# Optimization experiments

Hardware: AMD Instinct MI355X
Metric: run time of the kernel (lower is better)

## Reference

```python
import jax, jax.numpy as jnp
import numpy as np

VOCAB, EMB, H = 50000, 300, 64  # fgian_config: embed_dim=300, hidden_dim=64
POL = 3


def _lstm(x, lens, Wih, Whh, b):
    """Masked unidirectional LSTM (PyTorch gate order i,f,g,o).
    x: [B,T,D]; outputs zero past each sequence's length (packed-LSTM semantics)."""
    B, T, _ = x.shape
    Hh = Whh.shape[1]
    xs = jnp.einsum('btd,gd->btg', x, Wih) + b  # precompute input projection [B,T,4H]

    def step(carry, inp):
        h, c = carry
        xproj, t = inp
        g = xproj + h @ Whh.T
        i, f, gg, o = jnp.split(g, 4, axis=-1)
        i = jax.nn.sigmoid(i); f = jax.nn.sigmoid(f)
        gg = jnp.tanh(gg); o = jax.nn.sigmoid(o)
        c_new = f * c + i * gg
        h_new = o * jnp.tanh(c_new)
        m = (t < lens)[:, None]
        return (jnp.where(m, h_new, h), jnp.where(m, c_new, c)), jnp.where(m, h_new, 0.0)

    h0 = jnp.zeros((B, Hh), x.dtype)
    _, out = jax.lax.scan(step, (h0, h0), (xs.transpose(1, 0, 2), jnp.arange(T)))
    return out.transpose(1, 0, 2)


def _bilstm(x, lens, Wih_f, Whh_f, b_f, Wih_b, Whh_b, b_b):
    B, T, _ = x.shape
    t = jnp.arange(T)
    fwd = _lstm(x, lens, Wih_f, Whh_f, b_f)
    # reverse each sequence within its valid length, run fwd scan, reverse back
    ridx = jnp.clip(lens[:, None] - 1 - t[None, :], 0)  # [B,T]
    x_rev = jnp.take_along_axis(x, ridx[..., None], axis=1)
    bwd_rev = _lstm(x_rev, lens, Wih_b, Whh_b, b_b)
    bwd = jnp.take_along_axis(bwd_rev, ridx[..., None], axis=1)
    bwd = jnp.where((t[None, :] < lens[:, None])[..., None], bwd, 0.0)
    return jnp.concatenate([fwd, bwd], axis=-1)  # [B,T,2H]


def setup_inputs() -> dict:
    key = jax.random.key(0)
    ks = jax.random.split(key, 20)
    s = 0.1
    d = {
        'body_idx': jax.random.randint(ks[0], (128, 512), 0, VOCAB),
        'pun_idx': jax.random.randint(ks[1], (128, 256), 0, VOCAB),
        'emb': jax.random.normal(ks[2], (VOCAB, EMB), jnp.float32) * s,
        'w_u': jax.random.normal(ks[15], (6 * H,), jnp.float32) * s,
        'Wd': jax.random.normal(ks[16], (POL, 4 * H), jnp.float32) * s,
        'bd': jnp.zeros((POL,), jnp.float32),
    }
    names = ['bWih_f', 'bWhh_f', 'bb_f', 'bWih_b', 'bWhh_b', 'bb_b',
             'pWih_f', 'pWhh_f', 'pb_f', 'pWih_b', 'pWhh_b', 'pb_b']
    shapes = [(4 * H, EMB), (4 * H, H), (4 * H,)] * 4
    for i, (n, sh) in enumerate(zip(names, shapes)):
        d[n] = jax.random.normal(ks[3 + i], sh, jnp.float32) * s
    return d


def reference(body_idx, pun_idx, emb,
              bWih_f, bWhh_f, bb_f, bWih_b, bWhh_b, bb_b,
              pWih_f, pWhh_f, pb_f, pWih_b, pWhh_b, pb_b,
              w_u, Wd, bd):
    body_len = jnp.sum(body_idx != 0, axis=1)
    pun_len = jnp.sum(pun_idx != 0, axis=1)
    body_M = _bilstm(emb[body_idx], body_len, bWih_f, bWhh_f, bb_f, bWih_b, bWhh_b, bb_b)  # [B,T,2H]
    pun_M = _bilstm(emb[pun_idx], pun_len, pWih_f, pWhh_f, pb_f, pWih_b, pWhh_b, pb_b)     # [B,P,2H]

    # alignment[b,i,j] = [body_i, pun_j, body_i*pun_j] . w_u  -> fully vectorized
    w1, w2, w3 = jnp.split(w_u, 3)
    align = (jnp.einsum('btd,d->bt', body_M, w1)[:, :, None]
             + jnp.einsum('bpd,d->bp', pun_M, w2)[:, None, :]
             + jnp.einsum('btd,bpd->btp', body_M * w3, pun_M))  # [B,T,P]

    att_b = jax.nn.softmax(align.max(axis=2), axis=1)  # [B,T]
    f_pun2body = jnp.einsum('btd,bt->bd', body_M, att_b)
    att_p = jax.nn.softmax(align.max(axis=1), axis=1)  # [B,P]
    f_body2pun = jnp.einsum('bp,bpd->bd', att_p, pun_M)

    feat = jnp.concatenate([f_pun2body, f_body2pun], axis=1)  # [B,4H]
    return feat @ Wd.T + bd
```

## Files before the change

kernel.cpp:

```cpp
#include <hip/hip_runtime.h>


#define B 128
#define TBODY 512
#define TPUN 256
#define EMB 300
#define EMBP 320
#define VOCAB 50000
#define HID 64
#define G4 256
#define NG 512
#define DM 128

typedef __attribute__((ext_vector_type(8))) short bf16x8;
typedef __attribute__((ext_vector_type(4))) float floatx4;
typedef unsigned short u16;

#define OFF_XPB   0u
#define OFF_XPP   134217728u
#define OFF_BODYM 201326592u
#define OFF_PUNM  234881024u
#define OFF_SMALL 251658240u
#define OFF_ABODY (OFF_XPB + 0u)
#define OFF_APUN  (OFF_XPB + 262144u)
#define OFF_MT    (OFF_XPB + 393216u)
#define OFF_MP    (OFF_XPB + 655360u)
#define OFF_COLP  (OFF_XPB + 786432u)
#define OFF_EMBB  OFF_BODYM
#define OFF_WCB   OFF_PUNM
#define OFF_WCP   (OFF_PUNM + 327680u)
#define OFF_BIASB (OFF_PUNM + 655360u)
#define OFF_BIASP (OFF_PUNM + 657408u)
#define OFF_LENS  OFF_SMALL
#define OFF_FEAT  (OFF_SMALL + 1024u)

__device__ inline u16 f2bf(float v) {
    unsigned int u = __float_as_uint(v);
    unsigned int r = (u + 0x7FFFu + ((u >> 16) & 1u)) >> 16;
    return (u16)r;
}

__device__ inline void gload_lds16(const void* g, void* l) {
    __builtin_amdgcn_global_load_lds(
        (const __attribute__((address_space(1))) unsigned int*)g,
        (__attribute__((address_space(3))) unsigned int*)l, 16, 0, 0);
}

#define QBC(v, gg) __int_as_float(__builtin_amdgcn_update_dpp( \
    0, __float_as_int(v), (gg) * 0x55, 0xF, 0xF, true))

__global__ __launch_bounds__(256) void k_lens(const int* __restrict__ bidx,
                                              const int* __restrict__ pidx,
                                              int* __restrict__ lens) {
    int j = blockIdx.x, tid = threadIdx.x;
    const int* src; int n;
    if (j < B) { src = bidx + (size_t)j * TBODY; n = TBODY; }
    else       { src = pidx + (size_t)(j - B) * TPUN; n = TPUN; }
    int c = 0;
    for (int t = tid; t < n; t += 256) c += (src[t] != 0) ? 1 : 0;
    for (int o = 32; o; o >>= 1) c += __shfl_xor(c, o, 64);
    __shared__ int red[4];
    if ((tid & 63) == 0) red[tid >> 6] = c;
    __syncthreads();
    if (tid == 0) lens[j] = red[0] + red[1] + red[2] + red[3];
}

__global__ __launch_bounds__(256) void k_prep_emb(const float* __restrict__ emb,
                                                  u16* __restrict__ embb) {
    int e4 = (blockIdx.x * 256 + threadIdx.x) * 4;
    int row = e4 / EMBP, d = e4 - row * EMBP;
    u16 o0 = 0, o1 = 0, o2 = 0, o3 = 0;
    if (d < EMB) {
        float4 v = *(const float4*)(emb + (size_t)row * EMB + d);
        o0 = f2bf(v.x); o1 = f2bf(v.y); o2 = f2bf(v.z); o3 = f2bf(v.w);
    }
    ushort4 o = {o0, o1, o2, o3};
    *(ushort4*)(embb + e4) = o;
}

__global__ __launch_bounds__(256) void k_prep_w(
    const float* __restrict__ bWih_f, const float* __restrict__ bWih_b,
    const float* __restrict__ bb_f, const float* __restrict__ bb_b,
    const float* __restrict__ pWih_f, const float* __restrict__ pWih_b,
    const float* __restrict__ pb_f, const float* __restrict__ pb_b,
    u16* __restrict__ Wcb, u16* __restrict__ Wcp,
    float* __restrict__ biasb, float* __restrict__ biasp) {
    int e = blockIdx.x * 256 + threadIdx.x;
    const int WSZ = NG * EMBP;
    if (e < WSZ) {
        int g = e / EMBP, d = e - g * EMBP;
        float v = 0.f;
        if (d < EMB) v = (g < G4) ? bWih_f[g * EMB + d] : bWih_b[(g - G4) * EMB + d];
        Wcb[e] = f2bf(v);
    } else if (e < 2 * WSZ) {
        int ee = e - WSZ;
        int g = ee / EMBP, d = ee - g * EMBP;
        float v = 0.f;
        if (d < EMB) v = (g < G4) ? pWih_f[g * EMB + d] : pWih_b[(g - G4) * EMB + d];
        Wcp[ee] = f2bf(v);
    } else if (e < 2 * WSZ + NG) {
        int g = e - 2 * WSZ;
        biasb[g] = (g < G4) ? bb_f[g] : bb_b[g - G4];
    } else if (e < 2 * WSZ + 2 * NG) {
        int g = e - 2 * WSZ - NG;
        biasp[g] = (g < G4) ? pb_f[g] : pb_b[g - G4];
    }
}

__global__ __launch_bounds__(256) void k_gemm(const int* __restrict__ idx,
                                              const u16* __restrict__ embb,
                                              const u16* __restrict__ Wc,
                                              const float* __restrict__ biasc,
                                              float* __restrict__ out) {
    __shared__ u16 As[128 * 32];
    __shared__ u16 Bs[128 * 32];
    int tid = threadIdx.x, wave = tid >> 6, lane = tid & 63;
    int m0 = blockIdx.x * 128, g0 = blockIdx.y * 128;

    const u16* agp[2]; const u16* bgp[2];
    u16* asd[2]; u16* bsd[2];
#pragma unroll
    for (int j = 0; j < 2; j++) {
        int rbase = wave * 32 + j * 16;
        int r = rbase + (lane >> 2);
        int clog = (lane & 3) ^ (r & 3);
        int arow = idx[m0 + r];
        agp[j] = embb + (size_t)arow * EMBP + clog * 8;
        bgp[j] = Wc + (size_t)(g0 + r) * EMBP + clog * 8;
        asd[j] = As + rbase * 32;
        bsd[j] = Bs + rbase * 32;
    }

    int l15 = lane & 15, quad = lane >> 4;
    int mt0 = (wave >> 1) * 4, nt0 = (wave & 1) * 4;
    const u16* ard[4]; const u16* brd[4];
#pragma unroll
    for (int a = 0; a < 4; a++) {
        int r = (mt0 + a) * 16 + l15;
        ard[a] = As + r * 32 + ((quad ^ (r & 3)) * 8);
        int n = (nt0 + a) * 16 + l15;
        brd[a] = Bs + n * 32 + ((quad ^ (n & 3)) * 8);
    }

    floatx4 acc[4][4];
#pragma unroll
    for (int a = 0; a < 4; a++)
#pragma unroll
        for (int c = 0; c < 4; c++) acc[a][c] = (floatx4){0.f, 0.f, 0.f, 0.f};

    for (int k0 = 0; k0 < EMBP; k0 += 32) {
#pragma unroll
        for (int j = 0; j < 2; j++) {
            gload_lds16(agp[j] + k0, asd[j]);
            gload_lds16(bgp[j] + k0, bsd[j]);
        }
        __syncthreads();
        bf16x8 af[4], bfr[4];
#pragma unroll
        for (int a = 0; a < 4; a++) { af[a] = *(const bf16x8*)ard[a]; bfr[a] = *(const bf16x8*)brd[a]; }
#pragma unroll
        for (int a = 0; a < 4; a++)
#pragma unroll
            for (int c = 0; c < 4; c++)
                acc[a][c] = __builtin_amdgcn_mfma_f32_16x16x32_bf16(af[a], bfr[c], acc[a][c], 0, 0, 0);
        __syncthreads();
    }

#pragma unroll
    for (int c = 0; c < 4; c++) {
        int gcol = g0 + (nt0 + c) * 16 + l15;
        float bv = biasc[gcol];
#pragma unroll
        for (int a = 0; a < 4; a++) {
            int row0 = m0 + (mt0 + a) * 16 + quad * 4;
#pragma unroll
            for (int rg = 0; rg < 4; rg++)
                out[(size_t)(row0 + rg) * NG + gcol] = acc[a][c][rg] + bv;
        }
    }
}

#define DECLWR(n) \
    float Wr##n##0, Wr##n##1, Wr##n##2, Wr##n##3; \
    { int qs_ = (((l16 - (n)) & 15) << 2); \
      Wr##n##0 = vw[qs_]; Wr##n##1 = vw[qs_ + 1]; \
      Wr##n##2 = vw[qs_ + 2]; Wr##n##3 = vw[qs_ + 3]; }
#define FMACD(ACC, H, W, N) \
    asm("v_fmac_f32_dpp %0, %1, %2 row_ror:" #N " row_mask:0xf bank_mask:0xf" \
        : "+v"(ACC) : "v"(H), "v"(W));
#define RORF(n) { \
    FMACD(a0, hq.x, Wr##n##0, n) FMACD(a1, hq.y, Wr##n##1, n) \
    FMACD(a2, hq.z, Wr##n##2, n) FMACD(a3, hq.w, Wr##n##3, n) }

#define SBODY(S, XR) { \
    int p_ = dir ? (len - 1 - (S)) : (S); \
    float xv = XR; \
    int pn_ = dir ? (len - 3 - (S)) : ((S) + 2); \
    pn_ = min(max(pn_, 0), T - 1); \
    XR = xg[(size_t)pn_ * NG]; \
    float4 hq = *(const float4*)(&hbuf[(S) & 1][l16 * 4]); \
    float a0 = xv, a1 = 0.f, a2 = 0.f, a3 = 0.f; \
    a0 = fmaf(hq.x, Wr00, a0); a1 = fmaf(hq.y, Wr01, a1); \
    a2 = fmaf(hq.z, Wr02, a2); a3 = fmaf(hq.w, Wr03, a3); \
    RORF(1)  RORF(2)  RORF(3)  RORF(4)  RORF(5) \
    RORF(6)  RORF(7)  RORF(8)  RORF(9)  RORF(10) \
    RORF(11) RORF(12) RORF(13) RORF(14) RORF(15) \
    float pre = (a0 + a1) + (a2 + a3); \
    bool isg = (g == 2); \
    float t_in = isg ? (2.f * pre) : (-pre); \
    float e_ = __expf(t_in); \
    float r_ = __builtin_amdgcn_rcpf(1.f + e_); \
    float val = isg ? fmaf(-2.f, r_, 1.f) : r_; \
    float vi = QBC(val, 0); \
    float vf = QBC(val, 1); \
    float vg = QBC(val, 2); \
    float vo = QBC(val, 3); \
    c = fmaf(vf, c, vi * vg); \
    float th = fmaf(-2.f, __builtin_amdgcn_rcpf(1.f + __expf(2.f * c)), 1.f); \
    float h = vo * th; \
    if (g == 0) { \
        hbuf[((S) & 1) ^ 1][u] = h; \
        outp[(size_t)p_ * DM + u] = h; \
    } \
    asm volatile("s_waitcnt lgkmcnt(0)\n\ts_barrier" ::: "memory"); }

__global__ __attribute__((amdgpu_flat_work_group_size(256, 256),
                          amdgpu_waves_per_eu(2, 2))) void k_scan(
    const float* __restrict__ xpB, const float* __restrict__ xpP,
    float* __restrict__ bodyM, float* __restrict__ punM,
    const int* __restrict__ lens,
    const float* __restrict__ bWhh_f, const float* __restrict__ bWhh_b,
    const float* __restrict__ pWhh_f, const float* __restrict__ pWhh_b) {
    int task = blockIdx.x, tid = threadIdx.x;
    int isPun = task >> 8;
    int sub = task & 255;
    int b = sub & 127, dir = sub >> 7;
    int T = isPun ? TPUN : TBODY;
    int len = lens[(isPun ? B : 0) + b];
    int w = tid >> 6, l = tid & 63;
    int g = l & 3, q = l >> 2;
    int u = w * 16 + q;
    int l16 = l & 15;
    const float* xp = (isPun ? xpP : xpB) + (size_t)b * T * NG + dir * G4;
    float* outp = (isPun ? punM : bodyM) + (size_t)b * T * DM + dir * HID;
    const float* Whh = isPun ? (dir ? pWhh_b : pWhh_f) : (dir ? bWhh_b : bWhh_f);

    const volatile float* vw = Whh + (size_t)(g * 64 + u) * 64;
    DECLWR(0)  DECLWR(1)  DECLWR(2)  DECLWR(3)
    DECLWR(4)  DECLWR(5)  DECLWR(6)  DECLWR(7)
    DECLWR(8)  DECLWR(9)  DECLWR(10) DECLWR(11)
    DECLWR(12) DECLWR(13) DECLWR(14) DECLWR(15)

    __shared__ __align__(16) float hbuf[2][64];
    if (tid < 64) hbuf[0][tid] = 0.f;
    __syncthreads();
    if (len <= 0) return;

    const float* xg = xp + g * 64 + u;
    float c = 0.f;
    int p0 = dir ? (len - 1) : 0;
    int p1 = dir ? (len - 2) : 1;
    p1 = min(max(p1, 0), T - 1);
    float xA = xg[(size_t)p0 * NG];
    float xB = xg[(size_t)p1 * NG];
    int s = 0;
    for (; s + 1 < len; s += 2) {
        SBODY(s, xA)
        SBODY(s + 1, xB)
    }
    if (s < len) { SBODY(s, xA) }
}

__global__ __launch_bounds__(256) void k_rowdot(const float* __restrict__ bodyM,
                                                const float* __restrict__ punM,
                                                const float* __restrict__ w_u,
                                                float* __restrict__ a_body,
                                                float* __restrict__ a_pun) {
    int wid = (blockIdx.x * 256 + threadIdx.x) >> 6;
    int lane = threadIdx.x & 63;
    const int NB = B * TBODY;
    const float* src; const float* wv; float* dst;
    if (wid < NB) { src = bodyM + (size_t)wid * DM; wv = w_u; dst = a_body + wid; }
    else { src = punM + (size_t)(wid - NB) * DM; wv = w_u + DM; dst = a_pun + (wid - NB); }
    float2 v = ((const float2*)src)[lane];
    float2 w = ((const float2*)wv)[lane];
    float s = v.x * w.x + v.y * w.y;
    for (int o = 32; o; o >>= 1) s += __shfl_xor(s, o, 64);
    if (lane == 0) *dst = s;
}

__global__ __launch_bounds__(256) void k_align(
    const float* __restrict__ bodyM, const float* __restrict__ punM,
    const float* __restrict__ a_body, const float* __restrict__ a_pun,
    const float* __restrict__ w_u,
    float* __restrict__ m_t, float* __restrict__ colpart) {
    __shared__ float bw[64 * 132];
    __shared__ float pu[64 * 132];
    __shared__ float colred[64 * 16];
    int tid = threadIdx.x;
    int tt = blockIdx.x, b = blockIdx.y;
    int t0 = tt * 64;
    int ti = tid >> 4, pi = tid & 15;
    const float* w3 = w_u + 2 * DM;
    const float* bsrc = bodyM + ((size_t)b * TBODY + t0) * DM;
#pragma unroll
    for (int j = 0; j < 8; j++) {
        int e = tid + 256 * j;
        int i = e >> 5, c4 = e & 31;
        float4 v = *(const float4*)(bsrc + i * DM + c4 * 4);
        float4 wv = *(const float4*)(w3 + c4 * 4);
        v.x *= wv.x; v.y *= wv.y; v.z *= wv.z; v.w *= wv.w;
        *(float4*)(bw + i * 132 + c4 * 4) = v;
    }
    float aB[4];
#pragma unroll
    for (int a = 0; a < 4; a++) aB[a] = a_body[(size_t)b * TBODY + t0 + ti * 4 + a];
    float mrun[4] = {-1e30f, -1e30f, -1e30f, -1e30f};
    for (int pc = 0; pc < 4; pc++) {
        __syncthreads();
        const float* psrc = punM + ((size_t)b * TPUN + pc * 64) * DM;
#pragma unroll
        for (int j = 0; j < 8; j++) {
            int e = tid + 256 * j;
            int i = e >> 5, c4 = e & 31;
            float4 v = *(const float4*)(psrc + i * DM + c4 * 4);
            *(float4*)(pu + i * 132 + c4 * 4) = v;
        }
        __syncthreads();
        float aP[4];
#pragma unroll
        for (int c = 0; c < 4; c++) aP[c] = a_pun[(size_t)b * TPUN + pc * 64 + pi * 4 + c];
        float C[4][4];
#pragma unroll
        for (int a = 0; a < 4; a++)
#pragma unroll
            for (int c = 0; c < 4; c++) C[a][c] = 0.f;
        for (int d4 = 0; d4 < 32; d4++) {
            float4 bq[4];
#pragma unroll
            for (int a = 0; a < 4; a++) bq[a] = *(const float4*)(bw + (ti * 4 + a) * 132 + d4 * 4);
            float4 pq[4];
#pragma unroll
            for (int c = 0; c < 4; c++) pq[c] = *(const float4*)(pu + (pi * 4 + c) * 132 + d4 * 4);
#pragma unroll
            for (int dd = 0; dd < 4; dd++) {
#pragma unroll
                for (int a = 0; a < 4; a++) {
                    float bvv = (dd == 0) ? bq[a].x : (dd == 1) ? bq[a].y : (dd == 2) ? bq[a].z : bq[a].w;
#pragma unroll
                    for (int c = 0; c < 4; c++) {
                        float pv = (dd == 0) ? pq[c].x : (dd == 1) ? pq[c].y : (dd == 2) ? pq[c].z : pq[c].w;
                        C[a][c] += bvv * pv;
                    }
                }
            }
        }
        float colv[4] = {-1e30f, -1e30f, -1e30f, -1e30f};
#pragma unroll
        for (int a = 0; a < 4; a++) {
            float rm = -1e30f;
#pragma unroll
            for (int c = 0; c < 4; c++) {
                float valv = C[a][c] + aB[a] + aP[c];
                rm = fmaxf(rm, valv);
                colv[c] = fmaxf(colv[c], valv);
            }
#pragma unroll
            for (int o = 1; o < 16; o <<= 1) rm = fmaxf(rm, __shfl_xor(rm, o, 64));
            mrun[a] = fmaxf(mrun[a], rm);
        }
#pragma unroll
        for (int c = 0; c < 4; c++) colred[(pi * 4 + c) * 16 + ti] = colv[c];
        __syncthreads();
        if (tid < 64) {
            float m = -1e30f;
#pragma unroll
            for (int k = 0; k < 16; k++) m = fmaxf(m, colred[tid * 16 + k]);
            colpart[((size_t)b * 8 + tt) * TPUN + pc * 64 + tid] = m;
        }
    }
    if (pi == 0) {
#pragma unroll
        for (int a = 0; a < 4; a++) m_t[(size_t)b * TBODY + t0 + ti * 4 + a] = mrun[a];
    }
}

__global__ __launch_bounds__(256) void k_colmax(const float* __restrict__ colpart,
                                                float* __restrict__ m_p) {
    int b = blockIdx.x, p = threadIdx.x;
    float m = -1e30f;
    for (int tt = 0; tt < 8; tt++) m = fmaxf(m, colpart[((size_t)b * 8 + tt) * TPUN + p]);
    m_p[(size_t)b * TPUN + p] = m;
}

__global__ __launch_bounds__(256) void k_feat(const float* __restrict__ bodyM,
                                              const float* __restrict__ punM,
                                              const float* __restrict__ m_t,
                                              const float* __restrict__ m_p,
                                              float* __restrict__ feat) {
    int bidx = blockIdx.x;
    int b = bidx & (B - 1), which = bidx >> 7;
    int n = which ? TPUN : TBODY;
    const float* sc = which ? (m_p + (size_t)b * TPUN) : (m_t + (size_t)b * TBODY);
    const float* src = which ? (punM + (size_t)b * TPUN * DM) : (bodyM + (size_t)b * TBODY * DM);
    float* dst = feat + (size_t)b * 256 + which * DM;
    int tid = threadIdx.x;
    __shared__ float e_lds[TBODY];
    __shared__ float red[8];
    __shared__ float red2[256];
    float mx = -1e30f;
    for (int t = tid; t < n; t += 256) mx = fmaxf(mx, sc[t]);
    for (int o = 32; o; o >>= 1) mx = fmaxf(mx, __shfl_xor(mx, o, 64));
    if ((tid & 63) == 0) red[tid >> 6] = mx;
    __syncthreads();
    mx = fmaxf(fmaxf(red[0], red[1]), fmaxf(red[2], red[3]));
    float se = 0.f;
    for (int t = tid; t < n; t += 256) {
        float ev = __expf(sc[t] - mx);
        e_lds[t] = ev;
        se += ev;
    }
    for (int o = 32; o; o >>= 1) se += __shfl_xor(se, o, 64);
    if ((tid & 63) == 0) red[4 + (tid >> 6)] = se;
    __syncthreads();
    se = red[4] + red[5] + red[6] + red[7];
    float inv = 1.f / se;
    int d = tid & 127, half = tid >> 7;
    float acc = 0.f;
    for (int t = half; t < n; t += 2) acc += e_lds[t] * src[(size_t)t * DM + d];
    red2[tid] = acc;
    __syncthreads();
    if (tid < DM) dst[tid] = (red2[tid] + red2[tid + 128]) * inv;
}

__global__ __launch_bounds__(256) void k_out(const float* __restrict__ feat,
                                             const float* __restrict__ Wd,
                                             const float* __restrict__ bd,
                                             float* __restrict__ outp) {
    int b = blockIdx.x, tid = threadIdx.x;
    float v = feat[(size_t)b * 256 + tid];
    __shared__ float red[12];
#pragma unroll
    for (int pol = 0; pol < 3; pol++) {
        float s = v * Wd[pol * 256 + tid];
        for (int o = 32; o; o >>= 1) s += __shfl_xor(s, o, 64);
        if ((tid & 63) == 0) red[pol * 4 + (tid >> 6)] = s;
    }
    __syncthreads();
    if (tid < 3) outp[b * 3 + tid] = red[tid * 4] + red[tid * 4 + 1] + red[tid * 4 + 2] + red[tid * 4 + 3] + bd[tid];
}

extern "C" void kernel_launch(void* const* d_in, const int* in_sizes, int n_in,
                              void* d_out, int out_size, void* d_ws, size_t ws_size,
                              hipStream_t stream) {
    const int* body_idx = (const int*)d_in[0];
    const int* pun_idx  = (const int*)d_in[1];
    const float* emb    = (const float*)d_in[2];
    const float* w_u    = (const float*)d_in[3];
    const float* Wd     = (const float*)d_in[4];
    const float* bd     = (const float*)d_in[5];
    const float* bWih_f = (const float*)d_in[6];
    const float* bWhh_f = (const float*)d_in[7];
    const float* bb_f   = (const float*)d_in[8];
    const float* bWih_b = (const float*)d_in[9];
    const float* bWhh_b = (const float*)d_in[10];
    const float* bb_b   = (const float*)d_in[11];
    const float* pWih_f = (const float*)d_in[12];
    const float* pWhh_f = (const float*)d_in[13];
    const float* pb_f   = (const float*)d_in[14];
    const float* pWih_b = (const float*)d_in[15];
    const float* pWhh_b = (const float*)d_in[16];
    const float* pb_b   = (const float*)d_in[17];

    char* ws = (char*)d_ws;
    float* xpB   = (float*)(ws + OFF_XPB);
    float* xpP   = (float*)(ws + OFF_XPP);
    float* bodyM = (float*)(ws + OFF_BODYM);
    float* punM  = (float*)(ws + OFF_PUNM);
    u16* embb    = (u16*)(ws + OFF_EMBB);
    u16* Wcb     = (u16*)(ws + OFF_WCB);
    u16* Wcp     = (u16*)(ws + OFF_WCP);
    float* biasb = (float*)(ws + OFF_BIASB);
    float* biasp = (float*)(ws + OFF_BIASP);
    int* lens    = (int*)(ws + OFF_LENS);
    float* a_body = (float*)(ws + OFF_ABODY);
    float* a_pun  = (float*)(ws + OFF_APUN);
    float* m_t    = (float*)(ws + OFF_MT);
    float* m_p    = (float*)(ws + OFF_MP);
    float* colpart = (float*)(ws + OFF_COLP);
    float* feat   = (float*)(ws + OFF_FEAT);
    float* outp   = (float*)d_out;

    k_lens<<<dim3(256), dim3(256), 0, stream>>>(body_idx, pun_idx, lens);
    k_prep_emb<<<dim3(15625), dim3(256), 0, stream>>>(emb, embb);
    k_prep_w<<<dim3(1284), dim3(256), 0, stream>>>(bWih_f, bWih_b, bb_f, bb_b,
                                                   pWih_f, pWih_b, pb_f, pb_b,
                                                   Wcb, Wcp, biasb, biasp);
    k_gemm<<<dim3(512, 4), dim3(256), 0, stream>>>(body_idx, embb, Wcb, biasb, xpB);
    k_gemm<<<dim3(256, 4), dim3(256), 0, stream>>>(pun_idx, embb, Wcp, biasp, xpP);
    hipMemsetAsync(ws + OFF_BODYM, 0, (size_t)(33554432u + 16777216u), stream);
    k_scan<<<dim3(512), dim3(256), 0, stream>>>(xpB, xpP, bodyM, punM, lens,
                                                bWhh_f, bWhh_b, pWhh_f, pWhh_b);
    k_rowdot<<<dim3(24576), dim3(256), 0, stream>>>(bodyM, punM, w_u, a_body, a_pun);
    k_align<<<dim3(8, 128), dim3(256), 0, stream>>>(bodyM, punM, a_body, a_pun, w_u, m_t, colpart);
    k_colmax<<<dim3(128), dim3(256), 0, stream>>>(colpart, m_p);
    k_feat<<<dim3(256), dim3(256), 0, stream>>>(bodyM, punM, m_t, m_p, feat);
    k_out<<<dim3(128), dim3(256), 0, stream>>>(feat, Wd, bd, outp);
}
```

Measured before the change: 613.7 us.

## Merge prep kernels, zero scan tails in-kernel, use packed FMA in align

The three preprocessing kernels (lens, embedding bf16 conversion, weight packing) become a single launch with block-range dispatch. The 50MB memset of the body/pun outputs is dropped, and the scan kernel now zeroes only the padded timesteps past each sequence's length. The align inner product switches to v_pk_fma_f32 via inline asm on float pairs, which halves the FMA instruction count but changes the summation order. Together these cut launch overhead and redundant memory writes, at the cost of uncoalesced serial zeroing in the scan tail.

```diff
diff --git a/kernel.cpp b/kernel.cpp
--- a/kernel.cpp
+++ b/kernel.cpp
@@ -14,6 +14,7 @@
 
 typedef __attribute__((ext_vector_type(8))) short bf16x8;
 typedef __attribute__((ext_vector_type(4))) float floatx4;
+typedef __attribute__((ext_vector_type(2))) float f32x2;
 typedef unsigned short u16;
 
 #define OFF_XPB   0u
@@ -48,62 +49,63 @@
 
 #define QBC(v, gg) __int_as_float(__builtin_amdgcn_update_dpp( \
     0, __float_as_int(v), (gg) * 0x55, 0xF, 0xF, true))
-
-__global__ __launch_bounds__(256) void k_lens(const int* __restrict__ bidx,
-                                              const int* __restrict__ pidx,
-                                              int* __restrict__ lens) {
-    int j = blockIdx.x, tid = threadIdx.x;
-    const int* src; int n;
-    if (j < B) { src = bidx + (size_t)j * TBODY; n = TBODY; }
-    else       { src = pidx + (size_t)(j - B) * TPUN; n = TPUN; }
-    int c = 0;
-    for (int t = tid; t < n; t += 256) c += (src[t] != 0) ? 1 : 0;
-    for (int o = 32; o; o >>= 1) c += __shfl_xor(c, o, 64);
-    __shared__ int red[4];
-    if ((tid & 63) == 0) red[tid >> 6] = c;
-    __syncthreads();
-    if (tid == 0) lens[j] = red[0] + red[1] + red[2] + red[3];
-}
-
-__global__ __launch_bounds__(256) void k_prep_emb(const float* __restrict__ emb,
-                                                  u16* __restrict__ embb) {
-    int e4 = (blockIdx.x * 256 + threadIdx.x) * 4;
-    int row = e4 / EMBP, d = e4 - row * EMBP;
-    u16 o0 = 0, o1 = 0, o2 = 0, o3 = 0;
-    if (d < EMB) {
-        float4 v = *(const float4*)(emb + (size_t)row * EMB + d);
-        o0 = f2bf(v.x); o1 = f2bf(v.y); o2 = f2bf(v.z); o3 = f2bf(v.w);
-    }
-    ushort4 o = {o0, o1, o2, o3};
-    *(ushort4*)(embb + e4) = o;
-}
-
-__global__ __launch_bounds__(256) void k_prep_w(
+#define PKFMA2(acc, a2, b2) \
+    asm("v_pk_fma_f32 %0, %1, %2, %0" : "+v"(acc) : "v"(a2), "v"(b2));
+
+__global__ __launch_bounds__(256) void k_prep(
+    const float* __restrict__ emb, u16* __restrict__ embb,
+    const int* __restrict__ bidx, const int* __restrict__ pidx,
+    int* __restrict__ lens,
     const float* __restrict__ bWih_f, const float* __restrict__ bWih_b,
     const float* __restrict__ bb_f, const float* __restrict__ bb_b,
     const float* __restrict__ pWih_f, const float* __restrict__ pWih_b,
     const float* __restrict__ pb_f, const float* __restrict__ pb_b,
     u16* __restrict__ Wcb, u16* __restrict__ Wcp,
     float* __restrict__ biasb, float* __restrict__ biasp) {
-    int e = blockIdx.x * 256 + threadIdx.x;
-    const int WSZ = NG * EMBP;
-    if (e < WSZ) {
-        int g = e / EMBP, d = e - g * EMBP;
-        float v = 0.f;
-        if (d < EMB) v = (g < G4) ? bWih_f[g * EMB + d] : bWih_b[(g - G4) * EMB + d];
-        Wcb[e] = f2bf(v);
-    } else if (e < 2 * WSZ) {
-        int ee = e - WSZ;
-        int g = ee / EMBP, d = ee - g * EMBP;
-        float v = 0.f;
-        if (d < EMB) v = (g < G4) ? pWih_f[g * EMB + d] : pWih_b[(g - G4) * EMB + d];
-        Wcp[ee] = f2bf(v);
-    } else if (e < 2 * WSZ + NG) {
-        int g = e - 2 * WSZ;
-        biasb[g] = (g < G4) ? bb_f[g] : bb_b[g - G4];
-    } else if (e < 2 * WSZ + 2 * NG) {
-        int g = e - 2 * WSZ - NG;
-        biasp[g] = (g < G4) ? pb_f[g] : pb_b[g - G4];
+    int blk = blockIdx.x, tid = threadIdx.x;
+    if (blk < 15625) {
+        int e4 = (blk * 256 + tid) * 4;
+        int row = e4 / EMBP, d = e4 - row * EMBP;
+        u16 o0 = 0, o1 = 0, o2 = 0, o3 = 0;
+        if (d < EMB) {
+            float4 v = *(const float4*)(emb + (size_t)row * EMB + d);
+            o0 = f2bf(v.x); o1 = f2bf(v.y); o2 = f2bf(v.z); o3 = f2bf(v.w);
+        }
+        ushort4 o = {o0, o1, o2, o3};
+        *(ushort4*)(embb + e4) = o;
+    } else if (blk < 15625 + 256) {
+        int j = blk - 15625;
+        const int* src; int n;
+        if (j < B) { src = bidx + (size_t)j * TBODY; n = TBODY; }
+        else       { src = pidx + (size_t)(j - B) * TPUN; n = TPUN; }
+        int c = 0;
+        for (int t = tid; t < n; t += 256) c += (src[t] != 0) ? 1 : 0;
+        for (int o = 32; o; o >>= 1) c += __shfl_xor(c, o, 64);
+        __shared__ int red[4];
+        if ((tid & 63) == 0) red[tid >> 6] = c;
+        __syncthreads();
+        if (tid == 0) lens[j] = red[0] + red[1] + red[2] + red[3];
+    } else {
+        int e = (blk - 15881) * 256 + tid;
+        const int WSZ = NG * EMBP;
+        if (e < WSZ) {
+            int g = e / EMBP, d = e - g * EMBP;
+            float v = 0.f;
+            if (d < EMB) v = (g < G4) ? bWih_f[g * EMB + d] : bWih_b[(g - G4) * EMB + d];
+            Wcb[e] = f2bf(v);
+        } else if (e < 2 * WSZ) {
+            int ee = e - WSZ;
+            int g = ee / EMBP, d = ee - g * EMBP;
+            float v = 0.f;
+            if (d < EMB) v = (g < G4) ? pWih_f[g * EMB + d] : pWih_b[(g - G4) * EMB + d];
+            Wcp[ee] = f2bf(v);
+        } else if (e < 2 * WSZ + NG) {
+            int g = e - 2 * WSZ;
+            biasb[g] = (g < G4) ? bb_f[g] : bb_b[g - G4];
+        } else if (e < 2 * WSZ + 2 * NG) {
+            int g = e - 2 * WSZ - NG;
+            biasp[g] = (g < G4) ? pb_f[g] : pb_b[g - G4];
+        }
     }
 }
 
@@ -254,21 +256,26 @@
     __shared__ __align__(16) float hbuf[2][64];
     if (tid < 64) hbuf[0][tid] = 0.f;
     __syncthreads();
-    if (len <= 0) return;
-
-    const float* xg = xp + g * 64 + u;
-    float c = 0.f;
-    int p0 = dir ? (len - 1) : 0;
-    int p1 = dir ? (len - 2) : 1;
-    p1 = min(max(p1, 0), T - 1);
-    float xA = xg[(size_t)p0 * NG];
-    float xB = xg[(size_t)p1 * NG];
-    int s = 0;
-    for (; s + 1 < len; s += 2) {
-        SBODY(s, xA)
-        SBODY(s + 1, xB)
-    }
-    if (s < len) { SBODY(s, xA) }
+
+    if (len > 0) {
+        const float* xg = xp + g * 64 + u;
+        float c = 0.f;
+        int p0 = dir ? (len - 1) : 0;
+        int p1 = dir ? (len - 2) : 1;
+        p1 = min(max(p1, 0), T - 1);
+        float xA = xg[(size_t)p0 * NG];
+        float xB = xg[(size_t)p1 * NG];
+        int s = 0;
+        for (; s + 1 < len; s += 2) {
+            SBODY(s, xA)
+            SBODY(s + 1, xB)
+        }
+        if (s < len) { SBODY(s, xA) }
+    }
+    if (g == 0) {
+        for (int p = max(len, 0); p < T; ++p)
+            outp[(size_t)p * DM + u] = 0.f;
+    }
 }
 
 __global__ __launch_bounds__(256) void k_rowdot(const float* __restrict__ bodyM,
@@ -330,11 +337,11 @@
         float aP[4];
 #pragma unroll
         for (int c = 0; c < 4; c++) aP[c] = a_pun[(size_t)b * TPUN + pc * 64 + pi * 4 + c];
-        float C[4][4];
+        f32x2 C2[4][4];
 #pragma unroll
         for (int a = 0; a < 4; a++)
 #pragma unroll
-            for (int c = 0; c < 4; c++) C[a][c] = 0.f;
+            for (int c = 0; c < 4; c++) C2[a][c] = (f32x2){0.f, 0.f};
         for (int d4 = 0; d4 < 32; d4++) {
             float4 bq[4];
 #pragma unroll
@@ -343,15 +350,15 @@
 #pragma unroll
             for (int c = 0; c < 4; c++) pq[c] = *(const float4*)(pu + (pi * 4 + c) * 132 + d4 * 4);
 #pragma unroll
-            for (int dd = 0; dd < 4; dd++) {
-#pragma unroll
-                for (int a = 0; a < 4; a++) {
-                    float bvv = (dd == 0) ? bq[a].x : (dd == 1) ? bq[a].y : (dd == 2) ? bq[a].z : bq[a].w;
-#pragma unroll
-                    for (int c = 0; c < 4; c++) {
-                        float pv = (dd == 0) ? pq[c].x : (dd == 1) ? pq[c].y : (dd == 2) ? pq[c].z : pq[c].w;
-                        C[a][c] += bvv * pv;
-                    }
+            for (int a = 0; a < 4; a++) {
+                f32x2 blo = {bq[a].x, bq[a].y};
+                f32x2 bhi = {bq[a].z, bq[a].w};
+#pragma unroll
+                for (int c = 0; c < 4; c++) {
+                    f32x2 plo = {pq[c].x, pq[c].y};
+                    f32x2 phi = {pq[c].z, pq[c].w};
+                    PKFMA2(C2[a][c], blo, plo)
+                    PKFMA2(C2[a][c], bhi, phi)
                 }
             }
         }
@@ -361,7 +368,7 @@
             float rm = -1e30f;
 #pragma unroll
             for (int c = 0; c < 4; c++) {
-                float valv = C[a][c] + aB[a] + aP[c];
+                float valv = (C2[a][c].x + C2[a][c].y) + aB[a] + aP[c];
                 rm = fmaxf(rm, valv);
                 colv[c] = fmaxf(colv[c], valv);
             }
@@ -491,14 +498,12 @@
     float* feat   = (float*)(ws + OFF_FEAT);
     float* outp   = (float*)d_out;
 
-    k_lens<<<dim3(256), dim3(256), 0, stream>>>(body_idx, pun_idx, lens);
-    k_prep_emb<<<dim3(15625), dim3(256), 0, stream>>>(emb, embb);
-    k_prep_w<<<dim3(1284), dim3(256), 0, stream>>>(bWih_f, bWih_b, bb_f, bb_b,
-                                                   pWih_f, pWih_b, pb_f, pb_b,
-                                                   Wcb, Wcp, biasb, biasp);
+    k_prep<<<dim3(17165), dim3(256), 0, stream>>>(
+        emb, embb, body_idx, pun_idx, lens,
+        bWih_f, bWih_b, bb_f, bb_b, pWih_f, pWih_b, pb_f, pb_b,
+        Wcb, Wcp, biasb, biasp);
     k_gemm<<<dim3(512, 4), dim3(256), 0, stream>>>(body_idx, embb, Wcb, biasb, xpB);
     k_gemm<<<dim3(256, 4), dim3(256), 0, stream>>>(pun_idx, embb, Wcp, biasp, xpP);
-    hipMemsetAsync(ws + OFF_BODYM, 0, (size_t)(33554432u + 16777216u), stream);
     k_scan<<<dim3(512), dim3(256), 0, stream>>>(xpB, xpP, bodyM, punM, lens,
                                                 bWhh_f, bWhh_b, pWhh_f, pWhh_b);
     k_rowdot<<<dim3(24576), dim3(256), 0, stream>>>(bodyM, punM, w_u, a_body, a_pun);
```

After: 592.9 us (median of 2 runs). 3.4% less time.
